# Kernel tuning notes

Measured on AMD Instinct MI355X. Metric: run time of the kernel, lower is better.

## Reference

```python
import jax, jax.numpy as jnp
import numpy as np

B, S, D = 4, 2048, 1024
H = 16
DK = D // H  # 64


def setup_inputs() -> dict:
    key = jax.random.key(0)
    k1, k2, k3 = jax.random.split(key, 3)
    std_qkv = (2.0 / (D + 3 * D)) ** 0.5
    std_o = (2.0 / (D + D)) ** 0.5
    x = jax.random.normal(k1, (B, S, D), dtype=jnp.float32)
    W_qkv = jax.random.normal(k2, (3 * D, D), dtype=jnp.float32) * std_qkv
    W_o = jax.random.normal(k3, (D, D), dtype=jnp.float32) * std_o
    return {"x": x, "W_qkv": W_qkv, "W_o": W_o}


def reference(x, W_qkv, W_o):
    b, s, d = x.shape
    # qkv projection: [b, s, 3*H*DK]
    qkv = jnp.einsum('bsd,ed->bse', x, W_qkv)
    # rearrange '(c h dk)' -> c, b, h, s, dk
    qkv = qkv.reshape(b, s, 3, H, DK)
    qkv = jnp.transpose(qkv, (2, 0, 3, 1, 4))  # [3, b, h, s, dk]
    q, k, v = qkv[0], qkv[1], qkv[2]
    # scaled dot product attention with causal mask
    scores = jnp.einsum('bhqd,bhkd->bhqk', q, k) / (DK ** 0.5)
    causal = jnp.tril(jnp.ones((s, s), dtype=bool))
    scores = jnp.where(causal, scores, -jnp.inf)
    probs = jax.nn.softmax(scores, axis=-1)
    heads = jnp.einsum('bhqk,bhkd->bhqd', probs, v)
    # merge heads: [b, s, H*DK]
    heads = jnp.transpose(heads, (0, 2, 1, 3)).reshape(b, s, H * DK)
    return jnp.einsum('bse,de->bsd', heads, W_o)
```

## Files before the change

kernel.cpp:

```cpp
#include <hip/hip_runtime.h>
#include <hip/hip_bf16.h>

#define BB 4
#define SS 2048
#define DD 1024
#define HH 16
#define DKK 64

typedef __bf16 bf16x8 __attribute__((ext_vector_type(8)));
typedef float floatx4 __attribute__((ext_vector_type(4)));

#if __has_builtin(__builtin_amdgcn_exp2f)
#define EXP2(x) __builtin_amdgcn_exp2f(x)
#else
#define EXP2(x) exp2f(x)
#endif

__device__ __forceinline__ float b2f(unsigned short u) {
    union { unsigned int i; float f; } c;
    c.i = ((unsigned int)u) << 16;
    return c.f;
}
__device__ __forceinline__ unsigned short f2b(float f) {
    unsigned int i = __float_as_uint(f);
    unsigned int r = (i + 0x7FFFu + ((i >> 16) & 1u)) >> 16;
    return (unsigned short)r;
}
__device__ __forceinline__ unsigned int pkpair(float a, float b) {
    unsigned int ia = (__float_as_uint(a) + 0x8000u) >> 16;
    unsigned int ib = (__float_as_uint(b) + 0x8000u) & 0xffff0000u;
    return ia | ib;
}

__device__ __forceinline__ void gload_lds16(const unsigned short* g,
                                            unsigned short* l) {
    __builtin_amdgcn_global_load_lds(
        (const __attribute__((address_space(1))) unsigned int*)g,
        (__attribute__((address_space(3))) unsigned int*)l, 16, 0, 0);
}

__global__ void cvt_f32_bf16(const float* __restrict__ in,
                             unsigned short* __restrict__ out, int n4) {
    int i = blockIdx.x * blockDim.x + threadIdx.x;
    if (i >= n4) return;
    float4 v = ((const float4*)in)[i];
    ushort4 o;
    o.x = f2b(v.x); o.y = f2b(v.y); o.z = f2b(v.z); o.w = f2b(v.w);
    ((ushort4*)out)[i] = o;
}

template <typename CT>
__global__ __launch_bounds__(512, 1) void gemm_nt_128x256(
    const unsigned short* __restrict__ A,
    const unsigned short* __restrict__ B,
    CT* __restrict__ C, int M, int N, int K) {
    extern __shared__ unsigned short lds[];

    const int tid  = threadIdx.x;
    const int lane = tid & 63;
    const int w    = tid >> 6;
    const int wmh  = w >> 2;
    const int wnq  = w & 3;

    const int m0 = blockIdx.x * 128;
    const int n0 = blockIdx.y * 256;

    const int row16 = lane & 15;
    const int part  = lane >> 4;
    const int rbase = part * 4;
    const int shr   = (row16 & 7) << 3;

    const int srow = tid >> 3;
    const int scol = ((tid & 7) * 8) ^ ((srow & 7) << 3);
    const unsigned short* Ag = A + (size_t)(m0 + srow) * K + scol;
    const unsigned short* Bg = B + (size_t)(n0 + srow) * K + scol;
    const int ldsw = w * 512;

    const int NT = K >> 6;
    floatx4 acc[4][4] = {};

#define STAGE_TILE(t)                                                    \
    {                                                                    \
        unsigned short* sb = lds + ((t) & 1) * 24576;                    \
        const size_t ko = (size_t)(t) * 64;                              \
        _Pragma("unroll") for (int r2 = 0; r2 < 2; ++r2)                 \
            gload_lds16(Ag + (size_t)(r2 * 64) * K + ko,                 \
                        sb + r2 * 4096 + ldsw);                          \
        _Pragma("unroll") for (int r2 = 0; r2 < 4; ++r2)                 \
            gload_lds16(Bg + (size_t)(r2 * 64) * K + ko,                 \
                        sb + 8192 + r2 * 4096 + ldsw);                   \
    }

    STAGE_TILE(0);

    bf16x8 bfr[4][2];
    for (int kt = 0; kt < NT; ++kt) {
        const unsigned short* Ab = lds + (kt & 1) * 24576;
        const unsigned short* Bb = Ab + 8192;
#pragma unroll
        for (int q = 0; q < 2; ++q) {
            if (q == 0) {
                if (kt + 1 < NT) {
                    STAGE_TILE(kt + 1);
                    asm volatile("s_waitcnt vmcnt(6)" ::: "memory");
                } else {
                    asm volatile("s_waitcnt vmcnt(0)" ::: "memory");
                }
                __builtin_amdgcn_sched_barrier(0);
                __builtin_amdgcn_s_barrier();
#pragma unroll
                for (int j = 0; j < 4; ++j)
#pragma unroll
                    for (int u = 0; u < 2; ++u)
                        bfr[j][u] = *(const bf16x8*)(
                            Bb + (wnq * 64 + j * 16 + row16) * 64 +
                            ((u * 32 + part * 8) ^ shr));
            }
            bf16x8 af[2][2];
#pragma unroll
            for (int i = 0; i < 2; ++i)
#pragma unroll
                for (int u = 0; u < 2; ++u)
                    af[i][u] = *(const bf16x8*)(
                        Ab + (wmh * 64 + (q * 2 + i) * 16 + row16) * 64 +
                        ((u * 32 + part * 8) ^ shr));
            __builtin_amdgcn_s_barrier();
            asm volatile("s_waitcnt lgkmcnt(0)" ::: "memory");
            __builtin_amdgcn_sched_barrier(0);
            __builtin_amdgcn_s_setprio(1);
#pragma unroll
            for (int i = 0; i < 2; ++i)
#pragma unroll
                for (int j = 0; j < 4; ++j)
#pragma unroll
                    for (int u = 0; u < 2; ++u)
                        acc[q * 2 + i][j] =
                            __builtin_amdgcn_mfma_f32_16x16x32_bf16(
                                af[i][u], bfr[j][u], acc[q * 2 + i][j],
                                0, 0, 0);
            __builtin_amdgcn_s_setprio(0);
            __builtin_amdgcn_sched_barrier(0);
            __builtin_amdgcn_s_barrier();
        }
    }
#undef STAGE_TILE

#pragma unroll
    for (int i = 0; i < 4; ++i) {
#pragma unroll
        for (int j = 0; j < 4; ++j) {
            const int row = m0 + wmh * 64 + i * 16 + rbase;
            const int col = n0 + wnq * 64 + j * 16 + row16;
#pragma unroll
            for (int r = 0; r < 4; ++r) {
                size_t idx = (size_t)(row + r) * N + col;
                if constexpr (sizeof(CT) == 2) C[idx] = f2b(acc[i][j][r]);
                else                           C[idx] = acc[i][j][r];
            }
        }
    }
}

__global__ void repack_kv(const unsigned short* __restrict__ qkv,
                          unsigned short* __restrict__ Kp,
                          unsigned short* __restrict__ Vt) {
    __shared__ unsigned short Vs[64][72];
    const int st = blockIdx.x, h = blockIdx.y, b = blockIdx.z;
    const int tid = threadIdx.x;
    const size_t base = ((size_t)((b * HH + h) * (SS / 64) + st)) * 4096;

#pragma unroll
    for (int p = 0; p < 2; ++p) {
        const int row = p * 32 + (tid >> 3);
        const int chunk = tid & 7;
        size_t src = (size_t)(b * SS + st * 64 + row) * (3 * DD) +
                     DD + h * DKK + chunk * 8;
        uint4 kv = *(const uint4*)(qkv + src);
        *(uint4*)(Kp + base + (chunk >> 2) * 2048 + row * 32 + (chunk & 3) * 8) = kv;
        uint4 vv = *(const uint4*)(qkv + src + DD);
        *(uint4*)&Vs[row][chunk * 8] = vv;
    }
    __syncthreads();
#pragma unroll
    for (int p = 0; p < 2; ++p) {
        const int dk = p * 32 + (tid >> 3);
        const int s8 = tid & 7;
        union { unsigned short u[8]; uint4 v; } pk;
#pragma unroll
        for (int j = 0; j < 8; ++j) pk.u[j] = Vs[s8 * 8 + j][dk];
        *(uint4*)(Vt + base + (s8 >> 2) * 2048 + dk * 32 + (s8 & 3) * 8) = pk.v;
    }
}

struct StripState {
    bf16x8 qf[2][2];
    floatx4 O[2][4];
    float mrow[2], lrow[2];
    int q0w;
};

__device__ __forceinline__ void strip_init(
    StripState& S, const unsigned short* __restrict__ qkv,
    int b, int h, int q0w, int row16, int part) {
    const float c1 = 0.180336884f;
    S.q0w = q0w;
#pragma unroll
    for (int qt = 0; qt < 2; ++qt) {
        S.mrow[qt] = -1e30f;
        S.lrow[qt] = 0.f;
#pragma unroll
        for (int dt = 0; dt < 4; ++dt) S.O[qt][dt] = floatx4{0, 0, 0, 0};
#pragma unroll
        for (int u = 0; u < 2; ++u) {
            const unsigned short* qp = qkv +
                (size_t)(b * SS + q0w + qt * 16 + row16) * (3 * DD) +
                h * DKK + u * 32 + part * 8;
            union { uint4 r; unsigned short us[8]; } raw;
            raw.r = *(const uint4*)qp;
            union { unsigned short us[8]; bf16x8 v; } sq;
#pragma unroll
            for (int j = 0; j < 8; ++j) sq.us[j] = f2b(b2f(raw.us[j]) * c1);
            S.qf[qt][u] = sq.v;
        }
    }
}

__device__ __forceinline__ void strip_tile(
    StripState& S, int k0, const bf16x8 kf[2][4], const bf16x8 vf[2][4],
    int row16, int part, int rbase) {
#pragma unroll
    for (int qt = 0; qt < 2; ++qt) {
        floatx4 sc[4] = {};
#pragma unroll
        for (int u = 0; u < 2; ++u)
#pragma unroll
            for (int kt = 0; kt < 4; ++kt)
                sc[kt] = __builtin_amdgcn_mfma_f32_16x16x32_bf16(
                    kf[u][kt], S.qf[qt][u], sc[kt], 0, 0, 0);

        const int qa = S.q0w + qt * 16 + row16;
        const bool full = (k0 + 63 <= S.q0w + qt * 16);
        float mx = -1e30f;
#pragma unroll
        for (int kt = 0; kt < 4; ++kt)
#pragma unroll
            for (int r = 0; r < 4; ++r) {
                float s = sc[kt][r];
                if (!full) {
                    int ka = k0 + kt * 16 + rbase + r;
                    s = (ka <= qa) ? s : -1e30f;
                }
                sc[kt][r] = s;
                mx = fmaxf(mx, s);
            }
        mx = fmaxf(mx, __shfl_xor(mx, 16));
        mx = fmaxf(mx, __shfl_xor(mx, 32));

        const bool resc = !__all(mx - S.mrow[qt] <= 8.f);
        float mnew = resc ? fmaxf(S.mrow[qt], mx) : S.mrow[qt];

        float ps = 0.f;
        unsigned int pk[4][2];
#pragma unroll
        for (int kt = 0; kt < 4; ++kt) {
            float e0 = EXP2(sc[kt][0] - mnew);
            float e1 = EXP2(sc[kt][1] - mnew);
            float e2 = EXP2(sc[kt][2] - mnew);
            float e3 = EXP2(sc[kt][3] - mnew);
            ps += (e0 + e1) + (e2 + e3);
            pk[kt][0] = pkpair(e0, e1);
            pk[kt][1] = pkpair(e2, e3);
        }
        ps += __shfl_xor(ps, 16);
        ps += __shfl_xor(ps, 32);
        if (resc) {
            float alpha = EXP2(S.mrow[qt] - mnew);
            S.lrow[qt] = S.lrow[qt] * alpha + ps;
            S.mrow[qt] = mnew;
#pragma unroll
            for (int dt = 0; dt < 4; ++dt) S.O[qt][dt] *= alpha;
        } else {
            S.lrow[qt] += ps;
        }

        const int l0 = row16 + ((part & 1) * 2 + 0) * 16;
        const int l1 = row16 + ((part & 1) * 2 + 1) * 16;
        const bool hi = (part >> 1);
#pragma unroll
        for (int u = 0; u < 2; ++u) {
            unsigned int lo00 = (unsigned int)__shfl((int)pk[2 * u][0], l0);
            unsigned int lo01 = (unsigned int)__shfl((int)pk[2 * u][1], l0);
            unsigned int lo10 = (unsigned int)__shfl((int)pk[2 * u][0], l1);
            unsigned int lo11 = (unsigned int)__shfl((int)pk[2 * u][1], l1);
            unsigned int hi00 = (unsigned int)__shfl((int)pk[2 * u + 1][0], l0);
            unsigned int hi01 = (unsigned int)__shfl((int)pk[2 * u + 1][1], l0);
            unsigned int hi10 = (unsigned int)__shfl((int)pk[2 * u + 1][0], l1);
            unsigned int hi11 = (unsigned int)__shfl((int)pk[2 * u + 1][1], l1);
            union { unsigned int u32[4]; bf16x8 v; } P;
            P.u32[0] = hi ? hi00 : lo00;
            P.u32[1] = hi ? hi01 : lo01;
            P.u32[2] = hi ? hi10 : lo10;
            P.u32[3] = hi ? hi11 : lo11;
#pragma unroll
            for (int dt = 0; dt < 4; ++dt)
                S.O[qt][dt] = __builtin_amdgcn_mfma_f32_16x16x32_bf16(
                    vf[u][dt], P.v, S.O[qt][dt], 0, 0, 0);
        }
    }
}

__device__ __forceinline__ void strip_store(
    StripState& S, unsigned short* __restrict__ heads,
    int b, int h, int row16, int rbase) {
#pragma unroll
    for (int qt = 0; qt < 2; ++qt) {
        float inv = 1.f / S.lrow[qt];
#pragma unroll
        for (int dt = 0; dt < 4; ++dt) {
            ushort4 o4;
            o4.x = f2b(S.O[qt][dt][0] * inv);
            o4.y = f2b(S.O[qt][dt][1] * inv);
            o4.z = f2b(S.O[qt][dt][2] * inv);
            o4.w = f2b(S.O[qt][dt][3] * inv);
            size_t base = (size_t)(b * SS + S.q0w + qt * 16 + row16) * DD +
                          h * DKK + dt * 16 + rbase;
            *(ushort4*)&heads[base] = o4;
        }
    }
}

__global__ __launch_bounds__(256, 2) void attn_mfma6(
    const unsigned short* __restrict__ qkv,
    const unsigned short* __restrict__ Kp,
    const unsigned short* __restrict__ Vt,
    unsigned short* __restrict__ heads) {
    const int tid  = threadIdx.x;
    const int lane = tid & 63;
    const int w    = tid >> 6;

    const int bx   = blockIdx.x;
    const int xcd  = bx & 7;
    const int slot = bx >> 3;
    const int pair = xcd * 8 + (slot >> 3);
    const int blk  = slot & 7;
    const int b = pair >> 4, h = pair & 15;

    const int jA = blk * 4 + w;
    const int jB = 63 - jA;
    const int ntA = jA / 2 + 1;
    const int ntB = jB / 2 + 1;

    const int row16 = lane & 15;
    const int part  = lane >> 4;
    const int rbase = part * 4;

    StripState SA, SB;
    strip_init(SA, qkv, b, h, jA * 32, row16, part);
    strip_init(SB, qkv, b, h, jB * 32, row16, part);

    const size_t tb = (size_t)pair * (SS / 64) * 4096;

    for (int t = 0; t < ntB; ++t) {
        const int k0 = t * 64;
        const unsigned short* kbase = Kp + tb + (size_t)t * 4096;
        const unsigned short* vbase = Vt + tb + (size_t)t * 4096;
        bf16x8 kf[2][4], vf[2][4];
#pragma unroll
        for (int u = 0; u < 2; ++u)
#pragma unroll
            for (int i = 0; i < 4; ++i) {
                kf[u][i] = *(const bf16x8*)(kbase + u * 2048 +
                                            (i * 16 + row16) * 32 + part * 8);
                vf[u][i] = *(const bf16x8*)(vbase + u * 2048 +
                                            (i * 16 + row16) * 32 + part * 8);
            }
        strip_tile(SB, k0, kf, vf, row16, part, rbase);
        if (t < ntA) strip_tile(SA, k0, kf, vf, row16, part, rbase);
    }

    strip_store(SA, heads, b, h, row16, rbase);
    strip_store(SB, heads, b, h, row16, rbase);
}

extern "C" void kernel_launch(void* const* d_in, const int* in_sizes, int n_in,
                              void* d_out, int out_size, void* d_ws,
                              size_t ws_size, hipStream_t stream) {
    const float* x    = (const float*)d_in[0];
    const float* Wqkv = (const float*)d_in[1];
    const float* Wo   = (const float*)d_in[2];
    float* out = (float*)d_out;

    const size_t NX  = (size_t)BB * SS * DD;
    const size_t NWQ = (size_t)3 * DD * DD;
    const size_t NWO = (size_t)DD * DD;
    const size_t NKV = (size_t)BB * HH * SS * DKK;

    unsigned short* xb     = (unsigned short*)d_ws;
    unsigned short* wqkvb  = xb + NX;
    unsigned short* wob    = wqkvb + NWQ;
    unsigned short* qkvb   = wob + NWO;
    unsigned short* headsb = qkvb + (size_t)BB * SS * 3 * DD;
    unsigned short* Kp     = headsb + NX;
    unsigned short* Vtp    = Kp + NKV;

    static bool attr_done = false;
    if (!attr_done) {
        hipFuncSetAttribute(
            reinterpret_cast<const void*>(&gemm_nt_128x256<unsigned short>),
            hipFuncAttributeMaxDynamicSharedMemorySize, 98304);
        hipFuncSetAttribute(
            reinterpret_cast<const void*>(&gemm_nt_128x256<float>),
            hipFuncAttributeMaxDynamicSharedMemorySize, 98304);
        attr_done = true;
    }

    cvt_f32_bf16<<<(int)(NX / 4 / 256), 256, 0, stream>>>(x, xb, (int)(NX / 4));
    cvt_f32_bf16<<<(int)(NWQ / 4 / 256), 256, 0, stream>>>(Wqkv, wqkvb, (int)(NWQ / 4));
    cvt_f32_bf16<<<(int)(NWO / 4 / 256), 256, 0, stream>>>(Wo, wob, (int)(NWO / 4));

    gemm_nt_128x256<unsigned short><<<dim3(BB * SS / 128, 3 * DD / 256), 512,
                                     98304, stream>>>(xb, wqkvb, qkvb,
                                                      BB * SS, 3 * DD, DD);

    repack_kv<<<dim3(SS / 64, HH, BB), 256, 0, stream>>>(qkvb, Kp, Vtp);

    attn_mfma6<<<dim3(512), 256, 0, stream>>>(qkvb, Kp, Vtp, headsb);

    gemm_nt_128x256<float><<<dim3(BB * SS / 128, DD / 256), 512, 98304,
                             stream>>>(headsb, wob, out, BB * SS, DD, DD);
}
```

Measured before the change: 267.1 us.

## Split attention KV range across warp pairs and merge partial softmax states

Each pair of query strips is now handled by two waves that divide the KV tile range at a balanced split point. The second wave writes its partial O, max and sum to shared memory, and the first merges them flash-decoding style before storing. This doubles the grid to 1024 blocks and raises launch bounds to 4 blocks per CU, aiming at more parallelism and better occupancy in the attention stage. The cost is extra shared memory, a block-wide sync and the merge arithmetic.

```diff
diff --git a/kernel.cpp b/kernel.cpp
--- a/kernel.cpp
+++ b/kernel.cpp
@@ -329,26 +329,61 @@
     }
 }
 
-__global__ __launch_bounds__(256, 2) void attn_mfma6(
+__device__ __forceinline__ void strip_dump(const StripState& S, float* mb) {
+#pragma unroll
+    for (int qt = 0; qt < 2; ++qt)
+#pragma unroll
+        for (int dt = 0; dt < 4; ++dt)
+            *(floatx4*)&mb[qt * 16 + dt * 4] = S.O[qt][dt];
+    mb[32] = S.mrow[0]; mb[33] = S.mrow[1];
+    mb[34] = S.lrow[0]; mb[35] = S.lrow[1];
+}
+__device__ __forceinline__ void strip_merge(StripState& S, const float* mb) {
+#pragma unroll
+    for (int qt = 0; qt < 2; ++qt) {
+        float m1 = mb[32 + qt], l1 = mb[34 + qt];
+        float m  = fmaxf(S.mrow[qt], m1);
+        float a0 = EXP2(S.mrow[qt] - m);
+        float a1 = EXP2(m1 - m);
+        S.lrow[qt] = S.lrow[qt] * a0 + l1 * a1;
+#pragma unroll
+        for (int dt = 0; dt < 4; ++dt) {
+            floatx4 o1 = *(const floatx4*)&mb[qt * 16 + dt * 4];
+            S.O[qt][dt] = S.O[qt][dt] * a0 + o1 * a1;
+        }
+        S.mrow[qt] = m;
+    }
+}
+
+__global__ __launch_bounds__(256, 4) void attn_mfma9(
     const unsigned short* __restrict__ qkv,
     const unsigned short* __restrict__ Kp,
     const unsigned short* __restrict__ Vt,
     unsigned short* __restrict__ heads) {
+    __shared__ float mbuf[2][64][76];
+
     const int tid  = threadIdx.x;
     const int lane = tid & 63;
     const int w    = tid >> 6;
+    const int half = w & 1;
+    const int pidx = w >> 1;
 
     const int bx   = blockIdx.x;
     const int xcd  = bx & 7;
     const int slot = bx >> 3;
-    const int pair = xcd * 8 + (slot >> 3);
-    const int blk  = slot & 7;
+    const int pair = xcd * 8 + (slot >> 4);
+    const int pblk = slot & 15;
     const int b = pair >> 4, h = pair & 15;
 
-    const int jA = blk * 4 + w;
-    const int jB = 63 - jA;
+    const int jA  = pblk * 2 + pidx;
+    const int jB  = 63 - jA;
     const int ntA = jA / 2 + 1;
     const int ntB = jB / 2 + 1;
+    const int c   = (ntA >= 8) ? 8 : (17 - ntA);
+
+    const int t0  = half ? c : 0;
+    const int t1  = half ? ntB : c;
+    const int tA1 = half ? ntA : ((c < ntA) ? c : ntA);
 
     const int row16 = lane & 15;
     const int part  = lane >> 4;
@@ -360,7 +395,7 @@
 
     const size_t tb = (size_t)pair * (SS / 64) * 4096;
 
-    for (int t = 0; t < ntB; ++t) {
+    for (int t = t0; t < t1; ++t) {
         const int k0 = t * 64;
         const unsigned short* kbase = Kp + tb + (size_t)t * 4096;
         const unsigned short* vbase = Vt + tb + (size_t)t * 4096;
@@ -375,11 +410,21 @@
                                             (i * 16 + row16) * 32 + part * 8);
             }
         strip_tile(SB, k0, kf, vf, row16, part, rbase);
-        if (t < ntA) strip_tile(SA, k0, kf, vf, row16, part, rbase);
-    }
-
-    strip_store(SA, heads, b, h, row16, rbase);
-    strip_store(SB, heads, b, h, row16, rbase);
+        if (t < tA1) strip_tile(SA, k0, kf, vf, row16, part, rbase);
+    }
+
+    float* mb = &mbuf[pidx][lane][0];
+    if (half) {
+        strip_dump(SA, mb);
+        strip_dump(SB, mb + 36);
+    }
+    __syncthreads();
+    if (!half) {
+        strip_merge(SA, mb);
+        strip_merge(SB, mb + 36);
+        strip_store(SA, heads, b, h, row16, rbase);
+        strip_store(SB, heads, b, h, row16, rbase);
+    }
 }
 
 extern "C" void kernel_launch(void* const* d_in, const int* in_sizes, int n_in,
@@ -424,7 +469,7 @@
 
     repack_kv<<<dim3(SS / 64, HH, BB), 256, 0, stream>>>(qkvb, Kp, Vtp);
 
-    attn_mfma6<<<dim3(512), 256, 0, stream>>>(qkvb, Kp, Vtp, headsb);
+    attn_mfma9<<<dim3(1024), 256, 0, stream>>>(qkvb, Kp, Vtp, headsb);
 
     gemm_nt_128x256<float><<<dim3(BB * SS / 128, DD / 256), 512, 98304,
                              stream>>>(headsb, wob, out, BB * SS, DD, DD);
```

Measured after the change: 653.6 us. +144.7%, slower.
